# Kernel optimization log

Measured on AMD Instinct MI355X. Metric: run time of the kernel, lower is better.

The kernel has to match this reference:

```python
import jax, jax.numpy as jnp
import numpy as np

B, M, N = 16, 1024, 4096
CIN, HID = 67, 128  # in_channels+3, hid_channels
BN_EPS = 1e-5


def setup_inputs() -> dict:
    key = jax.random.key(0)
    ks = jax.random.split(key, 13)
    inp = {
        "cent_feat": jax.random.normal(ks[0], (B, M, CIN), dtype=jnp.float32),
        "feat": jax.random.normal(ks[1], (B, N, CIN), dtype=jnp.float32),
        "mask": jax.random.uniform(ks[2], (B, M, N), dtype=jnp.float32),
        # Conv1d(k=1, bias=False) weights, xavier-normal-ish scale
        "Wq": jax.random.normal(ks[3], (HID, CIN), dtype=jnp.float32) * np.float32(np.sqrt(2.0 / (HID + CIN))),
        "Wk": jax.random.normal(ks[4], (HID, CIN), dtype=jnp.float32) * np.float32(np.sqrt(2.0 / (HID + CIN))),
        # BatchNorm1d params (inference form)
        "gq": jax.random.uniform(ks[5], (HID,), dtype=jnp.float32, minval=0.5, maxval=1.5),
        "bq": jax.random.normal(ks[6], (HID,), dtype=jnp.float32) * 0.1,
        "mq": jax.random.normal(ks[7], (HID,), dtype=jnp.float32) * 0.1,
        "vq": jax.random.uniform(ks[8], (HID,), dtype=jnp.float32, minval=0.5, maxval=1.5),
        "gk": jax.random.uniform(ks[9], (HID,), dtype=jnp.float32, minval=0.5, maxval=1.5),
        "bk": jax.random.normal(ks[10], (HID,), dtype=jnp.float32) * 0.1,
        "mk": jax.random.normal(ks[11], (HID,), dtype=jnp.float32) * 0.1,
        "vk": jax.random.uniform(ks[12], (HID,), dtype=jnp.float32, minval=0.5, maxval=1.5),
    }
    return inp


def _bn(x, g, b, m, v):
    # BatchNorm1d over channel dim (last axis here), inference form
    return (x - m) * (g / jnp.sqrt(v + BN_EPS)) + b


def _l1_normalize(x, axis):
    # torch F.normalize(p=1): x / max(||x||_1, 1e-12)
    return x / jnp.maximum(jnp.sum(jnp.abs(x), axis=axis, keepdims=True), 1e-12)


def reference(cent_feat, feat, mask, Wq, Wk, gq, bq, mq, vq, gk, bk, mk, vk):
    # Conv1x1 (1x1 conv = channel matmul) + BN, no activation
    q = _bn(jnp.einsum("bmc,hc->bmh", cent_feat, Wq), gq, bq, mq, vq)  # [B,M,H]
    k = _bn(jnp.einsum("bnc,hc->bnh", feat, Wk), gk, bk, mk, vk)       # [B,N,H]
    adj = jnp.einsum("bmh,bnh->bmn", q, k)                              # [B,M,N]
    adj = jnp.where(mask < 1e-9, jnp.float32(-1e9), adj)
    adj = jax.nn.softmax(adj, axis=-1)
    adj = jnp.sqrt(mask + 1e-9) * jnp.sqrt(adj + 1e-9) - 1e-9
    adj = _l1_normalize(adj, axis=1)
    adj = _l1_normalize(adj, axis=-1)
    return adj
```

## Files before the change

### kernel.cpp

```cpp
#include <hip/hip_runtime.h>
#include <hip/hip_fp16.h>

#define B_ 16
#define M_ 1024
#define N_ 4096
#define H_ 128
#define CIN_ 67

typedef _Float16 half8 __attribute__((ext_vector_type(8)));
typedef _Float16 half4_t __attribute__((ext_vector_type(4)));
typedef float f32x4 __attribute__((ext_vector_type(4)));

#define SPA 104

__global__ __launch_bounds__(256) void k_embed(
    const float* __restrict__ cent, const float* __restrict__ feat,
    const float* __restrict__ Wq, const float* __restrict__ Wk,
    const float* __restrict__ gq, const float* __restrict__ bq,
    const float* __restrict__ mq, const float* __restrict__ vq,
    const float* __restrict__ gk, const float* __restrict__ bk,
    const float* __restrict__ mk, const float* __restrict__ vk,
    __half* __restrict__ q16, __half* __restrict__ k16)
{
  __shared__ __align__(16) __half al[128 * SPA];
  __shared__ __align__(16) __half wl[128 * SPA];
  __shared__ float scl[128], shl[128];

  const int tid = threadIdx.x;
  const int wg  = blockIdx.x;
  const bool isq = (wg < 128);
  const int row0 = isq ? wg * 128 : (wg - 128) * 128;
  const float* in = isq ? cent : feat;
  const float* W  = isq ? Wq : Wk;
  const float* g  = isq ? gq : gk;
  const float* bb = isq ? bq : bk;
  const float* mm = isq ? mq : mk;
  const float* vv = isq ? vq : vk;
  __half* outp = isq ? q16 : k16;

  for (int i = tid; i < 128 * 29; i += 256) {
    int r = i / 29, c = 67 + (i - r * 29);
    al[r * SPA + c] = __float2half(0.f);
    wl[r * SPA + c] = __float2half(0.f);
  }
  for (int i = tid; i < 128 * CIN_; i += 256) {
    int r = i / CIN_, c = i - r * CIN_;
    al[r * SPA + c] = __float2half(in[(size_t)row0 * CIN_ + i]);
    wl[r * SPA + c] = __float2half(W[i]);
  }
  if (tid < 128) {
    float s = g[tid] * rsqrtf(vv[tid] + 1e-5f);
    scl[tid] = s;
    shl[tid] = bb[tid] - mm[tid] * s;
  }
  __syncthreads();

  const int lane = tid & 63, wv = tid >> 6;
  const int col = lane & 15, quad = lane >> 4;

  f32x4 acc[2][8];
#pragma unroll
  for (int ms = 0; ms < 2; ++ms)
#pragma unroll
    for (int ns = 0; ns < 8; ++ns) acc[ms][ns] = (f32x4){0.f, 0.f, 0.f, 0.f};

#pragma unroll
  for (int kk = 0; kk < 3; ++kk) {
    half8 af[2], bf[8];
#pragma unroll
    for (int ms = 0; ms < 2; ++ms)
      af[ms] = *(const half8*)&al[(wv * 32 + ms * 16 + col) * SPA + kk * 32 + quad * 8];
#pragma unroll
    for (int ns = 0; ns < 8; ++ns)
      bf[ns] = *(const half8*)&wl[(ns * 16 + col) * SPA + kk * 32 + quad * 8];
#pragma unroll
    for (int ms = 0; ms < 2; ++ms)
#pragma unroll
      for (int ns = 0; ns < 8; ++ns)
        acc[ms][ns] = __builtin_amdgcn_mfma_f32_16x16x32_f16(af[ms], bf[ns], acc[ms][ns], 0, 0, 0);
  }

#pragma unroll
  for (int ms = 0; ms < 2; ++ms)
#pragma unroll
    for (int reg = 0; reg < 4; ++reg) {
      int r = wv * 32 + ms * 16 + quad * 4 + reg;
#pragma unroll
      for (int ns = 0; ns < 8; ++ns) {
        int h = ns * 16 + col;
        float v = acc[ms][ns][reg] * scl[h] + shl[h];
        outp[(size_t)(row0 + r) * H_ + h] = __float2half(v);
      }
    }
}

#define SPB 136

__global__ __launch_bounds__(256, 2) void k_attn1(
    const __half* __restrict__ q16, const __half* __restrict__ k16,
    float* __restrict__ Z)
{
  __shared__ __align__(16) __half qa[128 * SPB];
  __shared__ __align__(16) __half ka[128 * SPB];

  const int tid = threadIdx.x;
  const int b = blockIdx.z, mt = blockIdx.y, ns = blockIdx.x;
  const int m0 = mt * 128;

  {
    const uint4* srcq = (const uint4*)(q16 + ((size_t)(b * M_) + m0) * H_);
    for (int i = tid; i < 2048; i += 256) {
      int r = i >> 4, c = i & 15;
      *(uint4*)&qa[r * SPB + c * 8] = srcq[i];
    }
  }

  const int lane = tid & 63, wv = tid >> 6;
  const int col = lane & 15, quad = lane >> 4;

  float zacc[8];
#pragma unroll
  for (int i = 0; i < 8; ++i) zacc[i] = 0.f;

  for (int t = 0; t < 8; ++t) {
    if (t) __syncthreads();
    const int n0 = (ns * 8 + t) * 128;
    {
      const uint4* srck = (const uint4*)(k16 + ((size_t)(b * N_) + n0) * H_);
      for (int i = tid; i < 2048; i += 256) {
        int r = i >> 4, c = i & 15;
        *(uint4*)&ka[r * SPB + c * 8] = srck[i];
      }
    }
    __syncthreads();

    f32x4 acc[2][8];
#pragma unroll
    for (int ms = 0; ms < 2; ++ms)
#pragma unroll
      for (int nb = 0; nb < 8; ++nb) acc[ms][nb] = (f32x4){0.f, 0.f, 0.f, 0.f};

#pragma unroll
    for (int kk = 0; kk < 4; ++kk) {
      half8 af[2], bf[8];
#pragma unroll
      for (int ms = 0; ms < 2; ++ms)
        af[ms] = *(const half8*)&qa[(wv * 32 + ms * 16 + col) * SPB + kk * 32 + quad * 8];
#pragma unroll
      for (int nb = 0; nb < 8; ++nb)
        bf[nb] = *(const half8*)&ka[(nb * 16 + col) * SPB + kk * 32 + quad * 8];
#pragma unroll
      for (int ms = 0; ms < 2; ++ms)
#pragma unroll
        for (int nb = 0; nb < 8; ++nb)
          acc[ms][nb] = __builtin_amdgcn_mfma_f32_16x16x32_f16(af[ms], bf[nb], acc[ms][nb], 0, 0, 0);
    }

#pragma unroll
    for (int ms = 0; ms < 2; ++ms)
#pragma unroll
      for (int reg = 0; reg < 4; ++reg) {
        float s = 0.f;
#pragma unroll
        for (int nb = 0; nb < 8; ++nb) s += __expf(acc[ms][nb][reg]);
        zacc[ms * 4 + reg] += s;
      }
  }

#pragma unroll
  for (int i = 0; i < 8; ++i) {
    zacc[i] += __shfl_xor(zacc[i], 1);
    zacc[i] += __shfl_xor(zacc[i], 2);
    zacc[i] += __shfl_xor(zacc[i], 4);
    zacc[i] += __shfl_xor(zacc[i], 8);
  }
  if (col == 0) {
#pragma unroll
    for (int i = 0; i < 8; ++i) {
      int m = m0 + wv * 32 + (i >> 2) * 16 + quad * 4 + (i & 3);
      atomicAdd(&Z[(size_t)b * M_ + m], zacc[i]);
    }
  }
}

__global__ __launch_bounds__(256, 2) void k_attn3(
    const __half* __restrict__ q16, const __half* __restrict__ k16,
    const float* __restrict__ mask, const float* __restrict__ Z,
    __half* __restrict__ t16, float* __restrict__ colsum)
{
  __shared__ __align__(16) __half qa[128 * SPB];
  __shared__ __align__(16) __half ka[128 * SPB];
  __shared__ float lnZL[128];

  const int tid = threadIdx.x;
  const int b = blockIdx.z, mt = blockIdx.y, nt = blockIdx.x;
  const int m0 = mt * 128, n0 = nt * 128;

  {
    const uint4* srcq = (const uint4*)(q16 + ((size_t)(b * M_) + m0) * H_);
    const uint4* srck = (const uint4*)(k16 + ((size_t)(b * N_) + n0) * H_);
    for (int i = tid; i < 2048; i += 256) {
      int r = i >> 4, c = i & 15;
      *(uint4*)&qa[r * SPB + c * 8] = srcq[i];
      *(uint4*)&ka[r * SPB + c * 8] = srck[i];
    }
  }
  if (tid < 128) lnZL[tid] = __logf(Z[b * M_ + m0 + tid]);
  __syncthreads();

  const int lane = tid & 63, wv = tid >> 6;
  const int col = lane & 15, quad = lane >> 4;

  f32x4 acc[2][8];
#pragma unroll
  for (int ms = 0; ms < 2; ++ms)
#pragma unroll
    for (int ns = 0; ns < 8; ++ns) acc[ms][ns] = (f32x4){0.f, 0.f, 0.f, 0.f};

#pragma unroll
  for (int kk = 0; kk < 4; ++kk) {
    half8 af[2], bf[8];
#pragma unroll
    for (int ms = 0; ms < 2; ++ms)
      af[ms] = *(const half8*)&ka[(wv * 32 + ms * 16 + col) * SPB + kk * 32 + quad * 8];
#pragma unroll
    for (int ns = 0; ns < 8; ++ns)
      bf[ns] = *(const half8*)&qa[(ns * 16 + col) * SPB + kk * 32 + quad * 8];
#pragma unroll
    for (int ms = 0; ms < 2; ++ms)
#pragma unroll
      for (int ns = 0; ns < 8; ++ns)
        acc[ms][ns] = __builtin_amdgcn_mfma_f32_16x16x32_f16(af[ms], bf[ns], acc[ms][ns], 0, 0, 0);
  }

  float cs[8];
#pragma unroll
  for (int i = 0; i < 8; ++i) cs[i] = 0.f;

#pragma unroll
  for (int msN = 0; msN < 2; ++msN) {
    const int nb = n0 + wv * 32 + msN * 16 + quad * 4;
#pragma unroll
    for (int nsm = 0; nsm < 8; ++nsm) {
      const int ml = nsm * 16 + col;
      const int m = m0 + ml;
      const float lz = lnZL[ml];
      const size_t base = ((size_t)b * M_ + m) * N_ + nb;
      const float4 mv = *(const float4*)&mask[base];
      half4_t h;
#pragma unroll
      for (int reg = 0; reg < 4; ++reg) {
        float mvv = (reg == 0) ? mv.x : (reg == 1) ? mv.y : (reg == 2) ? mv.z : mv.w;
        float x = acc[msN][nsm][reg];
        x = (mvv < 1e-9f) ? -1e9f : x;
        float p = __expf(x - lz);
        float t = sqrtf((mvv + 1e-9f) * (p + 1e-9f)) - 1e-9f;
        h[reg] = (_Float16)t;
        cs[msN * 4 + reg] += t;
      }
      *(half4_t*)&t16[base] = h;
    }
  }
#pragma unroll
  for (int i = 0; i < 8; ++i) {
    cs[i] += __shfl_xor(cs[i], 1);
    cs[i] += __shfl_xor(cs[i], 2);
    cs[i] += __shfl_xor(cs[i], 4);
    cs[i] += __shfl_xor(cs[i], 8);
  }
  if (col == 0) {
#pragma unroll
    for (int i = 0; i < 8; ++i) {
      int n = n0 + wv * 32 + (i >> 2) * 16 + quad * 4 + (i & 3);
      atomicAdd(&colsum[(size_t)b * N_ + n], cs[i]);
    }
  }
}

__global__ __launch_bounds__(256) void k_norm(
    const __half* __restrict__ t16, float* __restrict__ out,
    const float* __restrict__ colsum)
{
  const int row = blockIdx.x;
  const int b = row >> 10;
  const half4_t* t4 = (const half4_t*)(t16 + (size_t)row * N_);
  float4* o4 = (float4*)(out + (size_t)row * N_);
  const float4* c4 = (const float4*)(colsum + (size_t)b * N_);
  const int tid = threadIdx.x;

  float4 u[4];
  float s = 0.f;
#pragma unroll
  for (int j = 0; j < 4; ++j) {
    int idx = tid + 256 * j;
    half4_t h = t4[idx];
    float4 c = c4[idx];
    u[j].x = (float)h[0] / fmaxf(c.x, 1e-12f);
    u[j].y = (float)h[1] / fmaxf(c.y, 1e-12f);
    u[j].z = (float)h[2] / fmaxf(c.z, 1e-12f);
    u[j].w = (float)h[3] / fmaxf(c.w, 1e-12f);
    s += u[j].x + u[j].y + u[j].z + u[j].w;
  }
  s += __shfl_xor(s, 1);
  s += __shfl_xor(s, 2);
  s += __shfl_xor(s, 4);
  s += __shfl_xor(s, 8);
  s += __shfl_xor(s, 16);
  s += __shfl_xor(s, 32);
  __shared__ float red[4];
  if ((tid & 63) == 0) red[tid >> 6] = s;
  __syncthreads();
  float tot = red[0] + red[1] + red[2] + red[3];
  float inv = 1.f / fmaxf(tot, 1e-12f);
#pragma unroll
  for (int j = 0; j < 4; ++j) {
    int idx = tid + 256 * j;
    float4 v = u[j];
    v.x *= inv; v.y *= inv; v.z *= inv; v.w *= inv;
    o4[idx] = v;
  }
}

extern "C" void kernel_launch(void* const* d_in, const int* in_sizes, int n_in,
                              void* d_out, int out_size, void* d_ws, size_t ws_size,
                              hipStream_t stream) {
  const float* cent = (const float*)d_in[0];
  const float* feat = (const float*)d_in[1];
  const float* mask = (const float*)d_in[2];
  const float* Wq = (const float*)d_in[3];
  const float* Wk = (const float*)d_in[4];
  const float* gq = (const float*)d_in[5];
  const float* bq = (const float*)d_in[6];
  const float* mq = (const float*)d_in[7];
  const float* vq = (const float*)d_in[8];
  const float* gk = (const float*)d_in[9];
  const float* bk = (const float*)d_in[10];
  const float* mk = (const float*)d_in[11];
  const float* vk = (const float*)d_in[12];
  float* out = (float*)d_out;

  char* ws = (char*)d_ws;
  __half* q16  = (__half*)(ws + 0);
  __half* k16  = (__half*)(ws + 4194304);
  __half* t16  = (__half*)(ws + 20971520);
  float* colsum= (float*)(ws + 155189248);
  float* Zr    = (float*)(ws + 155451392);

  hipMemsetAsync(colsum, 0, 262144 + 65536, stream);

  k_embed<<<640, 256, 0, stream>>>(cent, feat, Wq, Wk, gq, bq, mq, vq,
                                   gk, bk, mk, vk, q16, k16);

  dim3 g1(4, 8, 16);
  k_attn1<<<g1, 256, 0, stream>>>(q16, k16, Zr);

  dim3 g3(N_ / 128, M_ / 128, B_);
  k_attn3<<<g3, 256, 0, stream>>>(q16, k16, mask, Zr, t16, colsum);
  k_norm<<<B_ * M_, 256, 0, stream>>>(t16, out, colsum);
}
```

Baseline: 613.7 us.

## Prefetch K tiles into registers, hoist mask loads, precompute inverse column sums

In k_attn1 the next K tile is loaded into registers while the current tile is computed, so global-load latency overlaps the MFMA work. In k_attn3 all mask float4 loads are issued before the MFMA loop, so their latency hides behind the matmul. A small new kernel converts the column sums to reciprocals once, so k_norm multiplies instead of dividing per element. The trade-offs are higher register pressure (8 uint4 and 16 float4 held live), which may reduce occupancy, and one extra kernel launch.

```diff
diff --git a/kernel.cpp b/kernel.cpp
--- a/kernel.cpp
+++ b/kernel.cpp
@@ -107,12 +107,16 @@
   const int b = blockIdx.z, mt = blockIdx.y, ns = blockIdx.x;
   const int m0 = mt * 128;
 
+  uint4 kreg[8];
   {
     const uint4* srcq = (const uint4*)(q16 + ((size_t)(b * M_) + m0) * H_);
     for (int i = tid; i < 2048; i += 256) {
       int r = i >> 4, c = i & 15;
       *(uint4*)&qa[r * SPB + c * 8] = srcq[i];
     }
+    const uint4* srck0 = (const uint4*)(k16 + ((size_t)(b * N_) + ns * 8 * 128) * H_);
+#pragma unroll
+    for (int j = 0; j < 8; ++j) kreg[j] = srck0[tid + 256 * j];
   }
 
   const int lane = tid & 63, wv = tid >> 6;
@@ -124,15 +128,18 @@
 
   for (int t = 0; t < 8; ++t) {
     if (t) __syncthreads();
-    const int n0 = (ns * 8 + t) * 128;
-    {
-      const uint4* srck = (const uint4*)(k16 + ((size_t)(b * N_) + n0) * H_);
-      for (int i = tid; i < 2048; i += 256) {
-        int r = i >> 4, c = i & 15;
-        *(uint4*)&ka[r * SPB + c * 8] = srck[i];
-      }
+#pragma unroll
+    for (int j = 0; j < 8; ++j) {
+      int i = tid + 256 * j;
+      int r = i >> 4, c = i & 15;
+      *(uint4*)&ka[r * SPB + c * 8] = kreg[j];
     }
     __syncthreads();
+    if (t < 7) {
+      const uint4* srck = (const uint4*)(k16 + ((size_t)(b * N_) + (ns * 8 + t + 1) * 128) * H_);
+#pragma unroll
+      for (int j = 0; j < 8; ++j) kreg[j] = srck[tid + 256 * j];
+    }
 
     f32x4 acc[2][8];
 #pragma unroll
@@ -211,6 +218,17 @@
   const int lane = tid & 63, wv = tid >> 6;
   const int col = lane & 15, quad = lane >> 4;
 
+  float4 mv_[2][8];
+#pragma unroll
+  for (int msN = 0; msN < 2; ++msN) {
+    const int nb = n0 + wv * 32 + msN * 16 + quad * 4;
+#pragma unroll
+    for (int nsm = 0; nsm < 8; ++nsm) {
+      const int ml = nsm * 16 + col;
+      mv_[msN][nsm] = *(const float4*)&mask[((size_t)b * M_ + m0 + ml) * N_ + nb];
+    }
+  }
+
   f32x4 acc[2][8];
 #pragma unroll
   for (int ms = 0; ms < 2; ++ms)
@@ -246,7 +264,7 @@
       const int m = m0 + ml;
       const float lz = lnZL[ml];
       const size_t base = ((size_t)b * M_ + m) * N_ + nb;
-      const float4 mv = *(const float4*)&mask[base];
+      const float4 mv = mv_[msN][nsm];
       half4_t h;
 #pragma unroll
       for (int reg = 0; reg < 4; ++reg) {
@@ -277,15 +295,21 @@
   }
 }
 
+__global__ __launch_bounds__(256) void k_icol(float* __restrict__ cs)
+{
+  int i = blockIdx.x * 256 + threadIdx.x;
+  cs[i] = 1.f / fmaxf(cs[i], 1e-12f);
+}
+
 __global__ __launch_bounds__(256) void k_norm(
     const __half* __restrict__ t16, float* __restrict__ out,
-    const float* __restrict__ colsum)
+    const float* __restrict__ icol)
 {
   const int row = blockIdx.x;
   const int b = row >> 10;
   const half4_t* t4 = (const half4_t*)(t16 + (size_t)row * N_);
   float4* o4 = (float4*)(out + (size_t)row * N_);
-  const float4* c4 = (const float4*)(colsum + (size_t)b * N_);
+  const float4* c4 = (const float4*)(icol + (size_t)b * N_);
   const int tid = threadIdx.x;
 
   float4 u[4];
@@ -295,10 +319,10 @@
     int idx = tid + 256 * j;
     half4_t h = t4[idx];
     float4 c = c4[idx];
-    u[j].x = (float)h[0] / fmaxf(c.x, 1e-12f);
-    u[j].y = (float)h[1] / fmaxf(c.y, 1e-12f);
-    u[j].z = (float)h[2] / fmaxf(c.z, 1e-12f);
-    u[j].w = (float)h[3] / fmaxf(c.w, 1e-12f);
+    u[j].x = (float)h[0] * c.x;
+    u[j].y = (float)h[1] * c.y;
+    u[j].z = (float)h[2] * c.z;
+    u[j].w = (float)h[3] * c.w;
     s += u[j].x + u[j].y + u[j].z + u[j].w;
   }
   s += __shfl_xor(s, 1);
@@ -356,5 +380,6 @@
 
   dim3 g3(N_ / 128, M_ / 128, B_);
   k_attn3<<<g3, 256, 0, stream>>>(q16, k16, mask, Zr, t16, colsum);
+  k_icol<<<B_ * N_ / 256, 256, 0, stream>>>(colsum);
   k_norm<<<B_ * M_, 256, 0, stream>>>(t16, out, colsum);
 }
```

Result: no change. 623.0 us (+1.5%).

## Load MFMA operands straight from global into registers, drop LDS staging

Applied to the files above, without the earlier changes.

The two attention GEMM kernels stop staging Q/K tiles in shared memory. Each wave now loads its own fragments into registers straight from global memory, double-buffering the B fragments across the four K-steps. This removes the LDS writes and barriers and raises the occupancy hint to 3 blocks per SM. k_attn1 now uses twice as many blocks, each doing half as many tiles. A small kernel precomputes reciprocal column sums so the normalization kernel multiplies instead of dividing. The cost is redundant global/L2 fragment loads across waves, plus one extra kernel launch.

```diff
diff --git a/kernel.cpp b/kernel.cpp
--- a/kernel.cpp
+++ b/kernel.cpp
@@ -94,45 +94,50 @@
     }
 }
 
-#define SPB 136
-
-__global__ __launch_bounds__(256, 2) void k_attn1(
+#define A1_STEP(KK, CUR, NXT, PRE)                                          \
+  {                                                                         \
+    if (PRE) {                                                              \
+      _Pragma("unroll")                                                     \
+      for (int nb = 0; nb < 8; ++nb)                                        \
+        NXT[nb] = *(const half8*)(kt + (size_t)(nb * 16 + col) * H_ +       \
+                                  ((KK) + 1) * 32 + quad * 8);              \
+    }                                                                       \
+    _Pragma("unroll")                                                       \
+    for (int ms = 0; ms < 2; ++ms)                                          \
+      _Pragma("unroll")                                                     \
+      for (int nb = 0; nb < 8; ++nb)                                        \
+        acc[ms][nb] = __builtin_amdgcn_mfma_f32_16x16x32_f16(               \
+            qf[KK][ms], CUR[nb], acc[ms][nb], 0, 0, 0);                     \
+  }
+
+__global__ __launch_bounds__(256, 3) void k_attn1(
     const __half* __restrict__ q16, const __half* __restrict__ k16,
     float* __restrict__ Z)
 {
-  __shared__ __align__(16) __half qa[128 * SPB];
-  __shared__ __align__(16) __half ka[128 * SPB];
-
   const int tid = threadIdx.x;
   const int b = blockIdx.z, mt = blockIdx.y, ns = blockIdx.x;
   const int m0 = mt * 128;
-
-  {
-    const uint4* srcq = (const uint4*)(q16 + ((size_t)(b * M_) + m0) * H_);
-    for (int i = tid; i < 2048; i += 256) {
-      int r = i >> 4, c = i & 15;
-      *(uint4*)&qa[r * SPB + c * 8] = srcq[i];
-    }
-  }
-
   const int lane = tid & 63, wv = tid >> 6;
   const int col = lane & 15, quad = lane >> 4;
 
+  half8 qf[4][2];
+  {
+    const __half* qb = q16 + ((size_t)(b * M_) + m0 + wv * 32 + col) * H_;
+#pragma unroll
+    for (int kk = 0; kk < 4; ++kk)
+#pragma unroll
+      for (int ms = 0; ms < 2; ++ms)
+        qf[kk][ms] = *(const half8*)(qb + (size_t)ms * 16 * H_ + kk * 32 + quad * 8);
+  }
+
   float zacc[8];
 #pragma unroll
   for (int i = 0; i < 8; ++i) zacc[i] = 0.f;
 
-  for (int t = 0; t < 8; ++t) {
-    if (t) __syncthreads();
-    const int n0 = (ns * 8 + t) * 128;
-    {
-      const uint4* srck = (const uint4*)(k16 + ((size_t)(b * N_) + n0) * H_);
-      for (int i = tid; i < 2048; i += 256) {
-        int r = i >> 4, c = i & 15;
-        *(uint4*)&ka[r * SPB + c * 8] = srck[i];
-      }
-    }
-    __syncthreads();
+  const __half* kstrip = k16 + ((size_t)(b * N_) + ns * 512) * H_;
+
+  for (int t = 0; t < 4; ++t) {
+    const __half* kt = kstrip + (size_t)t * 128 * H_;
 
     f32x4 acc[2][8];
 #pragma unroll
@@ -140,21 +145,15 @@
 #pragma unroll
       for (int nb = 0; nb < 8; ++nb) acc[ms][nb] = (f32x4){0.f, 0.f, 0.f, 0.f};
 
-#pragma unroll
-    for (int kk = 0; kk < 4; ++kk) {
-      half8 af[2], bf[8];
-#pragma unroll
-      for (int ms = 0; ms < 2; ++ms)
-        af[ms] = *(const half8*)&qa[(wv * 32 + ms * 16 + col) * SPB + kk * 32 + quad * 8];
-#pragma unroll
-      for (int nb = 0; nb < 8; ++nb)
-        bf[nb] = *(const half8*)&ka[(nb * 16 + col) * SPB + kk * 32 + quad * 8];
-#pragma unroll
-      for (int ms = 0; ms < 2; ++ms)
-#pragma unroll
-        for (int nb = 0; nb < 8; ++nb)
-          acc[ms][nb] = __builtin_amdgcn_mfma_f32_16x16x32_f16(af[ms], bf[nb], acc[ms][nb], 0, 0, 0);
-    }
+    half8 bfA[8], bfB[8];
+#pragma unroll
+    for (int nb = 0; nb < 8; ++nb)
+      bfA[nb] = *(const half8*)(kt + (size_t)(nb * 16 + col) * H_ + quad * 8);
+
+    A1_STEP(0, bfA, bfB, 1)
+    A1_STEP(1, bfB, bfA, 1)
+    A1_STEP(2, bfA, bfB, 1)
+    A1_STEP(3, bfB, bfA, 0)
 
 #pragma unroll
     for (int ms = 0; ms < 2; ++ms)
@@ -183,55 +182,64 @@
   }
 }
 
-__global__ __launch_bounds__(256, 2) void k_attn3(
+#define A3_STEP(KK, CUR, NXT, PRE)                                          \
+  {                                                                         \
+    if (PRE) {                                                              \
+      _Pragma("unroll")                                                     \
+      for (int nb = 0; nb < 8; ++nb)                                        \
+        NXT[nb] = *(const half8*)(qb + (size_t)(nb * 16 + col) * H_ +       \
+                                  ((KK) + 1) * 32 + quad * 8);              \
+    }                                                                       \
+    _Pragma("unroll")                                                       \
+    for (int ms = 0; ms < 2; ++ms)                                          \
+      _Pragma("unroll")                                                     \
+      for (int nb = 0; nb < 8; ++nb)                                        \
+        acc[ms][nb] = __builtin_amdgcn_mfma_f32_16x16x32_f16(               \
+            kf[KK][ms], CUR[nb], acc[ms][nb], 0, 0, 0);                     \
+  }
+
+__global__ __launch_bounds__(256, 3) void k_attn3(
     const __half* __restrict__ q16, const __half* __restrict__ k16,
     const float* __restrict__ mask, const float* __restrict__ Z,
     __half* __restrict__ t16, float* __restrict__ colsum)
 {
-  __shared__ __align__(16) __half qa[128 * SPB];
-  __shared__ __align__(16) __half ka[128 * SPB];
-  __shared__ float lnZL[128];
-
   const int tid = threadIdx.x;
   const int b = blockIdx.z, mt = blockIdx.y, nt = blockIdx.x;
   const int m0 = mt * 128, n0 = nt * 128;
-
-  {
-    const uint4* srcq = (const uint4*)(q16 + ((size_t)(b * M_) + m0) * H_);
-    const uint4* srck = (const uint4*)(k16 + ((size_t)(b * N_) + n0) * H_);
-    for (int i = tid; i < 2048; i += 256) {
-      int r = i >> 4, c = i & 15;
-      *(uint4*)&qa[r * SPB + c * 8] = srcq[i];
-      *(uint4*)&ka[r * SPB + c * 8] = srck[i];
-    }
-  }
-  if (tid < 128) lnZL[tid] = __logf(Z[b * M_ + m0 + tid]);
-  __syncthreads();
-
   const int lane = tid & 63, wv = tid >> 6;
   const int col = lane & 15, quad = lane >> 4;
 
+  half8 kf[4][2];
+  {
+    const __half* kb = k16 + ((size_t)(b * N_) + n0 + wv * 32 + col) * H_;
+#pragma unroll
+    for (int kk = 0; kk < 4; ++kk)
+#pragma unroll
+      for (int ms = 0; ms < 2; ++ms)
+        kf[kk][ms] = *(const half8*)(kb + (size_t)ms * 16 * H_ + kk * 32 + quad * 8);
+  }
+
+  float lz[8];
+#pragma unroll
+  for (int nsm = 0; nsm < 8; ++nsm)
+    lz[nsm] = __logf(Z[(size_t)b * M_ + m0 + nsm * 16 + col]);
+
   f32x4 acc[2][8];
 #pragma unroll
   for (int ms = 0; ms < 2; ++ms)
 #pragma unroll
-    for (int ns = 0; ns < 8; ++ns) acc[ms][ns] = (f32x4){0.f, 0.f, 0.f, 0.f};
-
-#pragma unroll
-  for (int kk = 0; kk < 4; ++kk) {
-    half8 af[2], bf[8];
-#pragma unroll
-    for (int ms = 0; ms < 2; ++ms)
-      af[ms] = *(const half8*)&ka[(wv * 32 + ms * 16 + col) * SPB + kk * 32 + quad * 8];
-#pragma unroll
-    for (int ns = 0; ns < 8; ++ns)
-      bf[ns] = *(const half8*)&qa[(ns * 16 + col) * SPB + kk * 32 + quad * 8];
-#pragma unroll
-    for (int ms = 0; ms < 2; ++ms)
-#pragma unroll
-      for (int ns = 0; ns < 8; ++ns)
-        acc[ms][ns] = __builtin_amdgcn_mfma_f32_16x16x32_f16(af[ms], bf[ns], acc[ms][ns], 0, 0, 0);
-  }
+    for (int nb = 0; nb < 8; ++nb) acc[ms][nb] = (f32x4){0.f, 0.f, 0.f, 0.f};
+
+  const __half* qb = q16 + ((size_t)(b * M_) + m0) * H_;
+  half8 bfA[8], bfB[8];
+#pragma unroll
+  for (int nb = 0; nb < 8; ++nb)
+    bfA[nb] = *(const half8*)(qb + (size_t)(nb * 16 + col) * H_ + quad * 8);
+
+  A3_STEP(0, bfA, bfB, 1)
+  A3_STEP(1, bfB, bfA, 1)
+  A3_STEP(2, bfA, bfB, 1)
+  A3_STEP(3, bfB, bfA, 0)
 
   float cs[8];
 #pragma unroll
@@ -244,7 +252,7 @@
     for (int nsm = 0; nsm < 8; ++nsm) {
       const int ml = nsm * 16 + col;
       const int m = m0 + ml;
-      const float lz = lnZL[ml];
+      const float lzv = lz[nsm];
       const size_t base = ((size_t)b * M_ + m) * N_ + nb;
       const float4 mv = *(const float4*)&mask[base];
       half4_t h;
@@ -253,7 +261,7 @@
         float mvv = (reg == 0) ? mv.x : (reg == 1) ? mv.y : (reg == 2) ? mv.z : mv.w;
         float x = acc[msN][nsm][reg];
         x = (mvv < 1e-9f) ? -1e9f : x;
-        float p = __expf(x - lz);
+        float p = __expf(x - lzv);
         float t = sqrtf((mvv + 1e-9f) * (p + 1e-9f)) - 1e-9f;
         h[reg] = (_Float16)t;
         cs[msN * 4 + reg] += t;
@@ -277,15 +285,21 @@
   }
 }
 
+__global__ __launch_bounds__(256) void k_icol(float* __restrict__ cs)
+{
+  int i = blockIdx.x * 256 + threadIdx.x;
+  cs[i] = 1.f / fmaxf(cs[i], 1e-12f);
+}
+
 __global__ __launch_bounds__(256) void k_norm(
     const __half* __restrict__ t16, float* __restrict__ out,
-    const float* __restrict__ colsum)
+    const float* __restrict__ icol)
 {
   const int row = blockIdx.x;
   const int b = row >> 10;
   const half4_t* t4 = (const half4_t*)(t16 + (size_t)row * N_);
   float4* o4 = (float4*)(out + (size_t)row * N_);
-  const float4* c4 = (const float4*)(colsum + (size_t)b * N_);
+  const float4* c4 = (const float4*)(icol + (size_t)b * N_);
   const int tid = threadIdx.x;
 
   float4 u[4];
@@ -295,10 +309,10 @@
     int idx = tid + 256 * j;
     half4_t h = t4[idx];
     float4 c = c4[idx];
-    u[j].x = (float)h[0] / fmaxf(c.x, 1e-12f);
-    u[j].y = (float)h[1] / fmaxf(c.y, 1e-12f);
-    u[j].z = (float)h[2] / fmaxf(c.z, 1e-12f);
-    u[j].w = (float)h[3] / fmaxf(c.w, 1e-12f);
+    u[j].x = (float)h[0] * c.x;
+    u[j].y = (float)h[1] * c.y;
+    u[j].z = (float)h[2] * c.z;
+    u[j].w = (float)h[3] * c.w;
     s += u[j].x + u[j].y + u[j].z + u[j].w;
   }
   s += __shfl_xor(s, 1);
@@ -351,10 +365,11 @@
   k_embed<<<640, 256, 0, stream>>>(cent, feat, Wq, Wk, gq, bq, mq, vq,
                                    gk, bk, mk, vk, q16, k16);
 
-  dim3 g1(4, 8, 16);
+  dim3 g1(8, 8, 16);
   k_attn1<<<g1, 256, 0, stream>>>(q16, k16, Zr);
 
   dim3 g3(N_ / 128, M_ / 128, B_);
   k_attn3<<<g3, 256, 0, stream>>>(q16, k16, mask, Zr, t16, colsum);
+  k_icol<<<B_ * N_ / 256, 256, 0, stream>>>(colsum);
   k_norm<<<B_ * M_, 256, 0, stream>>>(t16, out, colsum);
 }
```

Result: slower. 703.7 us (+14.7%).
